# Kernel tuning notes

Hardware: AMD Instinct MI355X
Metric: run time of the kernel (lower is better)

## Reference

```python
import jax, jax.numpy as jnp
import numpy as np

NUM_HEADS = 8


def setup_inputs() -> dict:
    key = jax.random.key(0)
    ks = jax.random.split(key, 6)
    B, E, L = 8, 256, 4096
    top_k = 256
    return {
        "query": jax.random.normal(ks[0], (B, E, L), jnp.float32),
        "keys": jax.random.normal(ks[1], (B, E, L), jnp.float32),
        "values": jax.random.normal(ks[2], (B, E, L), jnp.float32),
        "rand_token_ind": jax.random.randint(ks[3], (B, top_k), 0, L),
        "in_proj_weight": jax.random.normal(ks[4], (3 * E, E), jnp.float32) / np.float32(np.sqrt(E)),
        "in_proj_bias": jnp.zeros((3 * E,), jnp.float32),
        "out_proj_weight": jax.random.normal(ks[5], (E, E), jnp.float32) / np.float32(np.sqrt(E)),
        "out_proj_bias": jnp.zeros((E,), jnp.float32),
        "top_k": top_k,
    }


def _forward(query, keys, values, rand_token_ind, in_proj_weight, in_proj_bias,
             out_proj_weight, out_proj_bias, top_k):
    B, E, Lq = query.shape
    # flatten(2).transpose(-1,-2): channel-first -> [B, L, E]
    q = jnp.swapaxes(query, 1, 2)
    k = jnp.swapaxes(keys, 1, 2)
    v = jnp.swapaxes(values, 1, 2)

    # --- dist_to_random_Q_selection ---
    # random subset of queries, [B, S, E]
    Q_small = jnp.take_along_axis(q, rand_token_ind[:, :, None], axis=1)

    # running min over subset queries of L1 distance (avoids [B,Lk,S,D] blowup)
    def step(min_d, qs):  # qs: [B, E]
        d = jnp.sum(jnp.abs(k - qs[:, None, :]), axis=-1)  # [B, Lk]
        return jnp.minimum(min_d, d), None

    init = jnp.full((B, k.shape[1]), jnp.inf, dtype=k.dtype)
    min_d, _ = jax.lax.scan(step, init, jnp.swapaxes(Q_small, 0, 1))

    # top_k smallest distances, sorted ascending (torch largest=False, sorted=True)
    _, idx = jax.lax.top_k(-min_d, top_k)  # idx: [B, top_k]
    sk = jnp.take_along_axis(k, idx[:, :, None], axis=1)  # [B, top_k, E]
    sv = jnp.take_along_axis(v, idx[:, :, None], axis=1)

    # --- standard torch MultiheadAttention (batch_first) ---
    Wq, Wk, Wv = jnp.split(in_proj_weight, 3, axis=0)
    bq, bk, bv = jnp.split(in_proj_bias, 3, axis=0)
    hd = E // NUM_HEADS
    scale = hd ** -0.5

    def heads(x):
        return x.reshape(x.shape[0], x.shape[1], NUM_HEADS, hd)

    qh = heads(q @ Wq.T + bq) * scale      # [B, Lq, H, hd]
    kh = heads(sk @ Wk.T + bk)             # [B, K,  H, hd]
    vh = heads(sv @ Wv.T + bv)

    scores = jnp.einsum('bqhd,bkhd->bhqk', qh, kh)
    attn = jax.nn.softmax(scores, axis=-1)
    o = jnp.einsum('bhqk,bkhd->bqhd', attn, vh).reshape(B, Lq, E)
    out = o @ out_proj_weight.T + out_proj_bias  # [B, Lq, E]

    # transpose back to original [B, E, Lq] layout
    return jnp.swapaxes(out, 1, 2)


def reference(query, keys, values, rand_token_ind, in_proj_weight, in_proj_bias,
              out_proj_weight, out_proj_bias, top_k):
    return _forward(query, keys, values, rand_token_ind, in_proj_weight,
                    in_proj_bias, out_proj_weight, out_proj_bias, top_k)
```

## Files before the change

### kernel.cpp

```cpp
#include <hip/hip_runtime.h>
#include <math.h>

#define B_SZ   8
#define E_DIM  256
#define L_SEQ  4096
#define S_TOP  256
#define NHEAD  8
#define HD     32
#define NSPLIT 4
#define JSPL   8

typedef __attribute__((ext_vector_type(8))) short bf16x8;
typedef __attribute__((ext_vector_type(4))) float f32x4;

__device__ inline short f2bf(float x) {
    union { float f; unsigned u; } v; v.f = x;
    unsigned r = (v.u + 0x7fff + ((v.u >> 16) & 1)) >> 16;
    return (short)r;
}
__device__ inline float bf2f(short h) {
    union { unsigned u; float f; } c; c.u = ((unsigned)(unsigned short)h) << 16;
    return c.f;
}

__global__ __launch_bounds__(256) void k_prep(const float* __restrict__ query,
                                              const int* __restrict__ ind,
                                              const float* __restrict__ wq,
                                              const float* __restrict__ wo,
                                              float* __restrict__ qs_pack,
                                              short* __restrict__ wqhi,
                                              short* __restrict__ wqlo,
                                              short* __restrict__ wohi,
                                              short* __restrict__ wolo,
                                              short* __restrict__ qhi,
                                              short* __restrict__ qlo) {
    __shared__ float T[64][68];
    const int blk = blockIdx.x;
    if (blk < 2048) {
        int t = blk * 256 + threadIdx.x;
        int e = t & (E_DIM - 1);
        int s = (t >> 8) & (S_TOP - 1);
        int b = t >> 16;
        int idx = ind[b * S_TOP + s];
        qs_pack[t] = query[((size_t)b * E_DIM + e) * L_SEQ + idx];
        return;
    }
    if (blk >= 4096) {
        int t = (blk - 4096) * 256 + threadIdx.x;
        float xq = wq[t];
        short hq = f2bf(xq);
        wqhi[t] = hq;
        wqlo[t] = f2bf(xq - bf2f(hq));
        float xo = wo[t];
        short ho = f2bf(xo);
        wohi[t] = ho;
        wolo[t] = f2bf(xo - bf2f(ho));
        return;
    }
    const int idx = blk - 2048;
    const int b  = idx >> 8;
    const int e0 = ((idx >> 6) & 3) * 64;
    const int l0 = (idx & 63) * 64;
    const float* src = query + ((size_t)b * E_DIM + e0) * L_SEQ + l0;
#pragma unroll
    for (int r = 0; r < 4; ++r) {
        int i2 = threadIdx.x + 256 * r;
        int e = i2 >> 4, l4 = (i2 & 15) * 4;
        *(float4*)&T[e][l4] = *(const float4*)(src + (size_t)e * L_SEQ + l4);
    }
    __syncthreads();
    const int l  = threadIdx.x >> 2;
    const int ec = (threadIdx.x & 3) * 16;
    size_t dst = ((size_t)b * L_SEQ + l0 + l) * E_DIM + e0 + ec;
    bf16x8 h0, h1, lo0, lo1;
#pragma unroll
    for (int k = 0; k < 8; ++k) {
        float x = T[ec + k][l];
        short h = f2bf(x);
        h0[k] = h; lo0[k] = f2bf(x - bf2f(h));
    }
#pragma unroll
    for (int k = 0; k < 8; ++k) {
        float x = T[ec + 8 + k][l];
        short h = f2bf(x);
        h1[k] = h; lo1[k] = f2bf(x - bf2f(h));
    }
    *(bf16x8*)(qhi + dst)     = h0;
    *(bf16x8*)(qhi + dst + 8) = h1;
    *(bf16x8*)(qlo + dst)     = lo0;
    *(bf16x8*)(qlo + dst + 8) = lo1;
}

__global__ __launch_bounds__(256) void k_dist(const float* __restrict__ keys,
                                              const float* __restrict__ qs_pack,
                                              double* __restrict__ minpart) {
    const int b  = blockIdx.z;
    const int ss = blockIdx.y;
    const int l0 = blockIdx.x * 64;
    const int lid = threadIdx.x;
    const int tx = lid & 15;
    const int ty = lid >> 4;
    __shared__ float Ks[32][64];
    __shared__ float Qs[64][36];
    double (*red)[64] = (double(*)[64])&Ks[0][0];

    const float* kb = keys + (size_t)b * E_DIM * L_SEQ + l0;
    const float* qb = qs_pack + ((size_t)b * S_TOP + ss * 64) * E_DIM;

    double d[4][4];
#pragma unroll
    for (int i = 0; i < 4; ++i)
#pragma unroll
        for (int j = 0; j < 4; ++j) d[i][j] = 0.0;

    float4 pk[2], pq[2];
    {
#pragma unroll
        for (int r = 0; r < 2; ++r) {
            int f4 = lid + 256 * r;
            int e  = f4 >> 4, l4 = (f4 & 15) * 4;
            pk[r] = *(const float4*)(kb + (size_t)e * L_SEQ + l4);
            int s  = f4 >> 3, e4 = (f4 & 7) * 4;
            pq[r] = *(const float4*)(qb + (size_t)s * E_DIM + e4);
        }
    }

    for (int c0 = 0; c0 < E_DIM; c0 += 32) {
        __syncthreads();
#pragma unroll
        for (int r = 0; r < 2; ++r) {
            int f4 = lid + 256 * r;
            int e  = f4 >> 4, l4 = (f4 & 15) * 4;
            *(float4*)&Ks[e][l4] = pk[r];
            int s  = f4 >> 3, e4 = (f4 & 7) * 4;
            *(float4*)&Qs[s][e4] = pq[r];
        }
        __syncthreads();
        if (c0 + 32 < E_DIM) {
            const int cn = c0 + 32;
#pragma unroll
            for (int r = 0; r < 2; ++r) {
                int f4 = lid + 256 * r;
                int e  = f4 >> 4, l4 = (f4 & 15) * 4;
                pk[r] = *(const float4*)(kb + (size_t)(cn + e) * L_SEQ + l4);
                int s  = f4 >> 3, e4 = (f4 & 7) * 4;
                pq[r] = *(const float4*)(qb + (size_t)s * E_DIM + cn + e4);
            }
        }

        float cs[4][4] = {};
#pragma unroll
        for (int e4 = 0; e4 < 32; e4 += 4) {
            float qv[4][4];
#pragma unroll
            for (int j = 0; j < 4; ++j) {
                float4 q = *(const float4*)&Qs[ty * 4 + j][e4];
                qv[j][0] = q.x; qv[j][1] = q.y; qv[j][2] = q.z; qv[j][3] = q.w;
            }
#pragma unroll
            for (int ee = 0; ee < 4; ++ee) {
                float kv[4];
#pragma unroll
                for (int i = 0; i < 4; ++i) kv[i] = Ks[e4 + ee][tx * 4 + i];
#pragma unroll
                for (int i = 0; i < 4; ++i)
#pragma unroll
                    for (int j = 0; j < 4; ++j)
                        cs[i][j] += fabsf(kv[i] - qv[j][ee]);
            }
        }
#pragma unroll
        for (int i = 0; i < 4; ++i)
#pragma unroll
            for (int j = 0; j < 4; ++j) d[i][j] += (double)cs[i][j];
    }

    double md[4];
#pragma unroll
    for (int i = 0; i < 4; ++i) {
        double m = d[i][0];
        m = fmin(m, d[i][1]);
        m = fmin(m, d[i][2]);
        m = fmin(m, d[i][3]);
        md[i] = m;
    }
    __syncthreads();
#pragma unroll
    for (int i = 0; i < 4; ++i) red[ty][tx * 4 + i] = md[i];
    __syncthreads();
    if (lid < 64) {
        double m = red[0][lid];
#pragma unroll
        for (int t = 1; t < 16; ++t) m = fmin(m, red[t][lid]);
        minpart[((size_t)(b * NSPLIT + ss)) * L_SEQ + l0 + lid] = m;
    }
}

__global__ __launch_bounds__(256) void k_rankpart(const double* __restrict__ minpart,
                                                  int* __restrict__ rankpart) {
    const int b  = blockIdx.z;
    const int js = blockIdx.y;
    const int l  = blockIdx.x * 256 + threadIdx.x;
    __shared__ double sd[512];
    const double* mp = minpart + (size_t)b * NSPLIT * L_SEQ;
    for (int jj = threadIdx.x; jj < 512; jj += 256) {
        const int j = js * 512 + jj;
        double v = mp[j];
        v = fmin(v, mp[L_SEQ + j]);
        v = fmin(v, mp[2 * L_SEQ + j]);
        v = fmin(v, mp[3 * L_SEQ + j]);
        sd[jj] = v;
    }
    double dl = mp[l];
    dl = fmin(dl, mp[L_SEQ + l]);
    dl = fmin(dl, mp[2 * L_SEQ + l]);
    dl = fmin(dl, mp[3 * L_SEQ + l]);
    __syncthreads();
    const int jbase = js * 512;
    int rank = 0;
#pragma unroll 8
    for (int jj = 0; jj < 512; ++jj) {
        double dj = sd[jj];
        rank += (dj < dl) || (dj == dl && (jbase + jj) < l) ? 1 : 0;
    }
    rankpart[((size_t)(b * JSPL + js)) * L_SEQ + l] = rank;
}

__global__ __launch_bounds__(256) void k_sel(const int* __restrict__ rankpart,
                                             int* __restrict__ sel) {
    const int t = blockIdx.x * 256 + threadIdx.x;
    const int b = t >> 12;
    const int l = t & (L_SEQ - 1);
    int r = 0;
#pragma unroll
    for (int s = 0; s < JSPL; ++s)
        r += rankpart[((size_t)(b * JSPL + s)) * L_SEQ + l];
    if (r < S_TOP) sel[b * S_TOP + r] = l;
}

__global__ __launch_bounds__(256) void k_kvproj2(const float* __restrict__ keys,
                                                 const float* __restrict__ vals,
                                                 const int* __restrict__ sel,
                                                 const float* __restrict__ Wk,
                                                 const float* __restrict__ bk,
                                                 const float* __restrict__ Wv,
                                                 const float* __restrict__ bv,
                                                 short* __restrict__ khb,
                                                 short* __restrict__ vtb) {
    const int b  = blockIdx.z;
    const int f0 = blockIdx.x * 64;
    const int TR = blockIdx.y >> 2;
    const int k0 = (blockIdx.y & 3) * 64;
    const float* src  = TR ? vals : keys;
    const float* W    = TR ? Wv : Wk;
    const float* bias = TR ? bv : bk;
    const int tx = threadIdx.x, ty = threadIdx.y;
    const int lid = ty * 16 + tx;
    __shared__ float As[16][68];
    __shared__ float Ws[16][68];
    float c[4][4] = {};
    const float* sb = src + (size_t)b * E_DIM * L_SEQ;
    const int* selb = sel + b * S_TOP;
    for (int e0 = 0; e0 < E_DIM; e0 += 16) {
        {
            int e  = lid >> 4;
            int k4 = (lid & 15) * 4;
#pragma unroll
            for (int c2 = 0; c2 < 4; ++c2) {
                int kk = k4 + c2;
                As[e][kk] = sb[(size_t)(e0 + e) * L_SEQ + selb[k0 + kk]];
            }
        }
        {
            int f  = lid >> 2;
            int e4 = (lid & 3) * 4;
            float4 w = *(const float4*)(W + (size_t)(f0 + f) * E_DIM + e0 + e4);
            Ws[e4 + 0][f] = w.x; Ws[e4 + 1][f] = w.y;
            Ws[e4 + 2][f] = w.z; Ws[e4 + 3][f] = w.w;
        }
        __syncthreads();
#pragma unroll
        for (int e = 0; e < 16; ++e) {
            float4 a = *(const float4*)&As[e][ty * 4];
            float4 w = *(const float4*)&Ws[e][tx * 4];
            float av[4] = {a.x, a.y, a.z, a.w};
            float wv[4] = {w.x, w.y, w.z, w.w};
#pragma unroll
            for (int i = 0; i < 4; ++i)
#pragma unroll
                for (int j = 0; j < 4; ++j) c[i][j] += av[i] * wv[j];
        }
        __syncthreads();
    }
    if (TR == 0) {
#pragma unroll
        for (int i = 0; i < 4; ++i) {
            short4 o;
            o.x = f2bf(c[i][0] + bias[f0 + tx * 4 + 0]);
            o.y = f2bf(c[i][1] + bias[f0 + tx * 4 + 1]);
            o.z = f2bf(c[i][2] + bias[f0 + tx * 4 + 2]);
            o.w = f2bf(c[i][3] + bias[f0 + tx * 4 + 3]);
            *(short4*)(khb + ((size_t)b * S_TOP + k0 + ty * 4 + i) * E_DIM + f0 + tx * 4) = o;
        }
    } else {
#pragma unroll
        for (int j = 0; j < 4; ++j) {
            const float bvv = bias[f0 + tx * 4 + j];
            short4 o;
            o.x = f2bf(c[0][j] + bvv); o.y = f2bf(c[1][j] + bvv);
            o.z = f2bf(c[2][j] + bvv); o.w = f2bf(c[3][j] + bvv);
            *(short4*)(vtb + ((size_t)b * E_DIM + f0 + tx * 4 + j) * S_TOP + k0 + ty * 4) = o;
        }
    }
}

__global__ __launch_bounds__(256) void k_qgemm(const short* __restrict__ qhi,
                                               const short* __restrict__ qlo,
                                               const short* __restrict__ wqhi,
                                               const short* __restrict__ wqlo,
                                               const float* __restrict__ bias,
                                               short* __restrict__ qhb,
                                               float scale) {
    const int b  = blockIdx.z;
    const int f0 = blockIdx.x * 128;
    const int l0 = blockIdx.y * 128;
    const int lid  = threadIdx.x;
    const int wv   = lid >> 6;
    const int lane = lid & 63;
    const int quad = lane >> 4;
    const int m    = lane & 15;
    const int wf   = wv >> 1;
    const int wl   = wv & 1;

    __shared__ short Awh[128 * 40];
    __shared__ short Awl[128 * 40];
    __shared__ short Bqh[128 * 40];
    __shared__ short Bql[128 * 40];

    const short* wh_g = wqhi + (size_t)f0 * E_DIM;
    const short* wl_g = wqlo + (size_t)f0 * E_DIM;
    const short* qh_g = qhi + ((size_t)b * L_SEQ + l0) * E_DIM;
    const short* ql_g = qlo + ((size_t)b * L_SEQ + l0) * E_DIM;

    f32x4 acc[4][4];
    const f32x4 zero = {0.f, 0.f, 0.f, 0.f};
#pragma unroll
    for (int i = 0; i < 4; ++i)
#pragma unroll
        for (int j = 0; j < 4; ++j) acc[i][j] = zero;

    for (int k0 = 0; k0 < E_DIM; k0 += 32) {
        __syncthreads();
#pragma unroll
        for (int r = 0; r < 2; ++r) {
            int idx = lid + 256 * r;
            int row = idx >> 2;
            int kc  = (idx & 3) * 8;
            *(bf16x8*)&Awh[row * 40 + kc] = *(const bf16x8*)(wh_g + (size_t)row * E_DIM + k0 + kc);
            *(bf16x8*)&Awl[row * 40 + kc] = *(const bf16x8*)(wl_g + (size_t)row * E_DIM + k0 + kc);
            *(bf16x8*)&Bqh[row * 40 + kc] = *(const bf16x8*)(qh_g + (size_t)row * E_DIM + k0 + kc);
            *(bf16x8*)&Bql[row * 40 + kc] = *(const bf16x8*)(ql_g + (size_t)row * E_DIM + k0 + kc);
        }
        __syncthreads();

        bf16x8 ah[4], al[4], bh[4], bl[4];
#pragma unroll
        for (int tf = 0; tf < 4; ++tf) {
            int row = wf * 64 + tf * 16 + m;
            ah[tf] = *(const bf16x8*)&Awh[row * 40 + quad * 8];
            al[tf] = *(const bf16x8*)&Awl[row * 40 + quad * 8];
        }
#pragma unroll
        for (int tl = 0; tl < 4; ++tl) {
            int row = wl * 64 + tl * 16 + m;
            bh[tl] = *(const bf16x8*)&Bqh[row * 40 + quad * 8];
            bl[tl] = *(const bf16x8*)&Bql[row * 40 + quad * 8];
        }
#pragma unroll
        for (int tf = 0; tf < 4; ++tf)
#pragma unroll
            for (int tl = 0; tl < 4; ++tl) {
                acc[tf][tl] = __builtin_amdgcn_mfma_f32_16x16x32_bf16(al[tf], bh[tl], acc[tf][tl], 0, 0, 0);
                acc[tf][tl] = __builtin_amdgcn_mfma_f32_16x16x32_bf16(ah[tf], bl[tl], acc[tf][tl], 0, 0, 0);
                acc[tf][tl] = __builtin_amdgcn_mfma_f32_16x16x32_bf16(ah[tf], bh[tl], acc[tf][tl], 0, 0, 0);
            }
    }

#pragma unroll
    for (int tf = 0; tf < 4; ++tf) {
        const int fb = f0 + wf * 64 + tf * 16 + quad * 4;
        float bv0 = bias[fb + 0], bv1 = bias[fb + 1];
        float bv2 = bias[fb + 2], bv3 = bias[fb + 3];
#pragma unroll
        for (int tl = 0; tl < 4; ++tl) {
            const int l = l0 + wl * 64 + tl * 16 + m;
            short4 o;
            o.x = f2bf(scale * (acc[tf][tl][0] + bv0));
            o.y = f2bf(scale * (acc[tf][tl][1] + bv1));
            o.z = f2bf(scale * (acc[tf][tl][2] + bv2));
            o.w = f2bf(scale * (acc[tf][tl][3] + bv3));
            *(short4*)(qhb + ((size_t)b * L_SEQ + l) * E_DIM + fb) = o;
        }
    }
}

__global__ __launch_bounds__(256) void k_attn(const short* __restrict__ qhb,
                                              const short* __restrict__ khb,
                                              const short* __restrict__ vtb,
                                              short* __restrict__ ohi,
                                              short* __restrict__ olo) {
    __shared__ short P[4][16][264];
    const int b = blockIdx.z, h = blockIdx.y;
    const int wv   = threadIdx.x >> 6;
    const int lane = threadIdx.x & 63;
    const int quad = lane >> 4;
    const int m    = lane & 15;
    const int l0 = blockIdx.x * 64 + wv * 16;

    const short* qp = qhb + ((size_t)b * L_SEQ + l0 + m) * E_DIM + h * HD + quad * 8;
    const bf16x8 qa = *(const bf16x8*)qp;

    const short* kb = khb + (size_t)b * S_TOP * E_DIM + h * HD + quad * 8;
    f32x4 sacc[16];
    const f32x4 zero = {0.f, 0.f, 0.f, 0.f};
#pragma unroll
    for (int t = 0; t < 16; ++t) {
        bf16x8 kf = *(const bf16x8*)(kb + (size_t)(t * 16 + m) * E_DIM);
        sacc[t] = __builtin_amdgcn_mfma_f32_16x16x32_bf16(qa, kf, zero, 0, 0, 0);
    }

    float mx[4], ssum[4];
#pragma unroll
    for (int r = 0; r < 4; ++r) {
        float v = sacc[0][r];
#pragma unroll
        for (int t = 1; t < 16; ++t) v = fmaxf(v, sacc[t][r]);
#pragma unroll
        for (int off = 1; off < 16; off <<= 1) v = fmaxf(v, __shfl_xor(v, off, 16));
        mx[r] = v;
        ssum[r] = 0.f;
    }
#pragma unroll
    for (int t = 0; t < 16; ++t) {
#pragma unroll
        for (int r = 0; r < 4; ++r) {
            float p = __expf(sacc[t][r] - mx[r]);
            ssum[r] += p;
            P[wv][quad * 4 + r][t * 16 + m] = f2bf(p);
        }
    }
#pragma unroll
    for (int r = 0; r < 4; ++r) {
        float v = ssum[r];
#pragma unroll
        for (int off = 1; off < 16; off <<= 1) v += __shfl_xor(v, off, 16);
        ssum[r] = v;
    }

    const short* vb = vtb + ((size_t)b * E_DIM + h * HD) * S_TOP;
    f32x4 oacc[2];
#pragma unroll
    for (int dt = 0; dt < 2; ++dt) {
        f32x4 acc = zero;
#pragma unroll
        for (int k0 = 0; k0 < S_TOP; k0 += 32) {
            bf16x8 pa = *(const bf16x8*)&P[wv][m][k0 + quad * 8];
            bf16x8 vf = *(const bf16x8*)(vb + (size_t)(dt * 16 + m) * S_TOP + k0 + quad * 8);
            acc = __builtin_amdgcn_mfma_f32_16x16x32_bf16(pa, vf, acc, 0, 0, 0);
        }
        oacc[dt] = acc;
    }

    short* oph = ohi + ((size_t)b * L_SEQ + l0) * E_DIM + h * HD;
    short* opl = olo + ((size_t)b * L_SEQ + l0) * E_DIM + h * HD;
#pragma unroll
    for (int r = 0; r < 4; ++r) {
        const float inv = 1.0f / ssum[r];
#pragma unroll
        for (int dt = 0; dt < 2; ++dt) {
            float val = oacc[dt][r] * inv;
            short hh = f2bf(val);
            size_t off = (size_t)(quad * 4 + r) * E_DIM + dt * 16 + m;
            oph[off] = hh;
            opl[off] = f2bf(val - bf2f(hh));
        }
    }
}

__global__ __launch_bounds__(256) void k_ogemm(const short* __restrict__ ohi,
                                               const short* __restrict__ olo,
                                               const short* __restrict__ wohi,
                                               const short* __restrict__ wolo,
                                               const float* __restrict__ bias,
                                               float* __restrict__ out) {
    const int b  = blockIdx.z;
    const int f0 = blockIdx.x * 128;
    const int l0 = blockIdx.y * 128;
    const int lid  = threadIdx.x;
    const int wv   = lid >> 6;
    const int lane = lid & 63;
    const int quad = lane >> 4;
    const int m    = lane & 15;
    const int wl   = wv >> 1;
    const int wf   = wv & 1;

    __shared__ short Aoh[128 * 40];
    __shared__ short Aol[128 * 40];
    __shared__ short Bwh[128 * 40];
    __shared__ short Bwl[128 * 40];

    const short* oh_g = ohi + ((size_t)b * L_SEQ + l0) * E_DIM;
    const short* ol_g = olo + ((size_t)b * L_SEQ + l0) * E_DIM;
    const short* wh_g = wohi + (size_t)f0 * E_DIM;
    const short* wl_g = wolo + (size_t)f0 * E_DIM;

    f32x4 acc[4][4];
    const f32x4 zero = {0.f, 0.f, 0.f, 0.f};
#pragma unroll
    for (int i = 0; i < 4; ++i)
#pragma unroll
        for (int j = 0; j < 4; ++j) acc[i][j] = zero;

    for (int k0 = 0; k0 < E_DIM; k0 += 32) {
        __syncthreads();
#pragma unroll
        for (int r = 0; r < 2; ++r) {
            int idx = lid + 256 * r;
            int row = idx >> 2;
            int kc  = (idx & 3) * 8;
            *(bf16x8*)&Aoh[row * 40 + kc] = *(const bf16x8*)(oh_g + (size_t)row * E_DIM + k0 + kc);
            *(bf16x8*)&Aol[row * 40 + kc] = *(const bf16x8*)(ol_g + (size_t)row * E_DIM + k0 + kc);
            *(bf16x8*)&Bwh[row * 40 + kc] = *(const bf16x8*)(wh_g + (size_t)row * E_DIM + k0 + kc);
            *(bf16x8*)&Bwl[row * 40 + kc] = *(const bf16x8*)(wl_g + (size_t)row * E_DIM + k0 + kc);
        }
        __syncthreads();

        bf16x8 ah[4], al[4], bh[4], bl[4];
#pragma unroll
        for (int tl = 0; tl < 4; ++tl) {
            int row = wl * 64 + tl * 16 + m;
            ah[tl] = *(const bf16x8*)&Aoh[row * 40 + quad * 8];
            al[tl] = *(const bf16x8*)&Aol[row * 40 + quad * 8];
        }
#pragma unroll
        for (int tf = 0; tf < 4; ++tf) {
            int row = wf * 64 + tf * 16 + m;
            bh[tf] = *(const bf16x8*)&Bwh[row * 40 + quad * 8];
            bl[tf] = *(const bf16x8*)&Bwl[row * 40 + quad * 8];
        }
#pragma unroll
        for (int tl = 0; tl < 4; ++tl)
#pragma unroll
            for (int tf = 0; tf < 4; ++tf) {
                acc[tl][tf] = __builtin_amdgcn_mfma_f32_16x16x32_bf16(al[tl], bh[tf], acc[tl][tf], 0, 0, 0);
                acc[tl][tf] = __builtin_amdgcn_mfma_f32_16x16x32_bf16(ah[tl], bl[tf], acc[tl][tf], 0, 0, 0);
                acc[tl][tf] = __builtin_amdgcn_mfma_f32_16x16x32_bf16(ah[tl], bh[tf], acc[tl][tf], 0, 0, 0);
            }
    }

#pragma unroll
    for (int tl = 0; tl < 4; ++tl) {
        const int lb = l0 + wl * 64 + tl * 16 + quad * 4;
#pragma unroll
        for (int tf = 0; tf < 4; ++tf) {
            const int f = f0 + wf * 64 + tf * 16 + m;
            const float bv = bias[f];
            float4 o;
            o.x = acc[tl][tf][0] + bv;
            o.y = acc[tl][tf][1] + bv;
            o.z = acc[tl][tf][2] + bv;
            o.w = acc[tl][tf][3] + bv;
            *(float4*)(out + ((size_t)b * E_DIM + f) * L_SEQ + lb) = o;
        }
    }
}

extern "C" void kernel_launch(void* const* d_in, const int* in_sizes, int n_in,
                              void* d_out, int out_size, void* d_ws, size_t ws_size,
                              hipStream_t stream) {
    const float* query = (const float*)d_in[0];
    const float* keys  = (const float*)d_in[1];
    const float* vals  = (const float*)d_in[2];
    const int*   rind  = (const int*)d_in[3];
    const float* ipw   = (const float*)d_in[4];
    const float* ipb   = (const float*)d_in[5];
    const float* opw   = (const float*)d_in[6];
    const float* opb   = (const float*)d_in[7];
    float* out = (float*)d_out;

    char* ws = (char*)d_ws;
    const size_t MI = 1024 * 1024;
    float*  qs_pack  = (float*)(ws + 0);
    double* minpart  = (double*)(ws + 2 * MI);
    int*    sel      = (int*)   (ws + 3 * MI);
    short*  khb      = (short*) (ws + 4 * MI);
    int*    rankpart = (int*)   (ws + 5 * MI);
    short*  vtb      = (short*) (ws + 6 * MI);
    short*  wqhi     = (short*) (ws + 7 * MI);
    short*  wqlo     = (short*) (ws + 7 * MI + 131072);
    short*  wohi     = (short*) (ws + 7 * MI + 2 * 131072);
    short*  wolo     = (short*) (ws + 7 * MI + 3 * 131072);
    short*  qhb      = (short*) (ws + 8 * MI);
    short*  qhi      = (short*) (ws + 24 * MI);
    short*  qlo      = (short*) (ws + 40 * MI);
    short*  ohi      = (short*) (ws + 24 * MI);
    short*  olo      = (short*) (ws + 40 * MI);

    const float scale = 0.17677669529663687f;

    k_prep<<<dim3(4352), 256, 0, stream>>>(query, rind, ipw, opw, qs_pack,
                                           wqhi, wqlo, wohi, wolo, qhi, qlo);
    k_dist<<<dim3(L_SEQ / 64, NSPLIT, B_SZ), dim3(256), 0, stream>>>(keys, qs_pack, minpart);
    k_rankpart<<<dim3(L_SEQ / 256, JSPL, B_SZ), 256, 0, stream>>>(minpart, rankpart);
    k_sel<<<dim3((B_SZ * L_SEQ) / 256), 256, 0, stream>>>(rankpart, sel);
    k_kvproj2<<<dim3(E_DIM / 64, 2 * (S_TOP / 64), B_SZ), dim3(16, 16), 0, stream>>>(
        keys, vals, sel,
        ipw + (size_t)E_DIM * E_DIM, ipb + E_DIM,
        ipw + (size_t)2 * E_DIM * E_DIM, ipb + 2 * E_DIM,
        khb, vtb);
    k_qgemm<<<dim3(E_DIM / 128, L_SEQ / 128, B_SZ), 256, 0, stream>>>(
        qhi, qlo, wqhi, wqlo, ipb, qhb, scale);
    k_attn<<<dim3(L_SEQ / 64, NHEAD, B_SZ), 256, 0, stream>>>(qhb, khb, vtb, ohi, olo);
    k_ogemm<<<dim3(E_DIM / 128, L_SEQ / 128, B_SZ), 256, 0, stream>>>(
        ohi, olo, wohi, wolo, opb, out);
}
```

Measured before the change: 470.3 us.

## Double-buffer distance kernel tiles via direct global-to-LDS loads

The L1-distance kernel now loads key and query tiles straight into shared memory with global_load_lds, instead of staging them through registers. Shared memory is double-buffered so the next chunk's load is issued while the current chunk is computed. This cuts register pressure and the LDS store instructions. It drops the Qs padding, which may bring back bank conflicts. There is also no explicit wait on the async LDS writes beyond __syncthreads, so correctness depends on the compiler inserting vmcnt waits.

```diff
diff --git a/kernel.cpp b/kernel.cpp
--- a/kernel.cpp
+++ b/kernel.cpp
@@ -12,6 +12,10 @@
 
 typedef __attribute__((ext_vector_type(8))) short bf16x8;
 typedef __attribute__((ext_vector_type(4))) float f32x4;
+
+#define GLDS16(gsrc, ldst) __builtin_amdgcn_global_load_lds( \
+    (const __attribute__((address_space(1))) void*)(gsrc),   \
+    (__attribute__((address_space(3))) void*)(ldst), 16, 0, 0)
 
 __device__ inline short f2bf(float x) {
     union { float f; unsigned u; } v; v.f = x;
@@ -100,9 +104,9 @@
     const int lid = threadIdx.x;
     const int tx = lid & 15;
     const int ty = lid >> 4;
-    __shared__ float Ks[32][64];
-    __shared__ float Qs[64][36];
-    double (*red)[64] = (double(*)[64])&Ks[0][0];
+    __shared__ float Ks[2][32][64];
+    __shared__ float Qs[2][64][32];
+    double (*red)[64] = (double(*)[64])&Ks[0][0][0];
 
     const float* kb = keys + (size_t)b * E_DIM * L_SEQ + l0;
     const float* qb = qs_pack + ((size_t)b * S_TOP + ss * 64) * E_DIM;
@@ -113,38 +117,30 @@
 #pragma unroll
         for (int j = 0; j < 4; ++j) d[i][j] = 0.0;
 
-    float4 pk[2], pq[2];
     {
 #pragma unroll
         for (int r = 0; r < 2; ++r) {
             int f4 = lid + 256 * r;
             int e  = f4 >> 4, l4 = (f4 & 15) * 4;
-            pk[r] = *(const float4*)(kb + (size_t)e * L_SEQ + l4);
+            GLDS16(kb + (size_t)e * L_SEQ + l4, &Ks[0][e][l4]);
             int s  = f4 >> 3, e4 = (f4 & 7) * 4;
-            pq[r] = *(const float4*)(qb + (size_t)s * E_DIM + e4);
-        }
-    }
-
-    for (int c0 = 0; c0 < E_DIM; c0 += 32) {
-        __syncthreads();
-#pragma unroll
-        for (int r = 0; r < 2; ++r) {
-            int f4 = lid + 256 * r;
-            int e  = f4 >> 4, l4 = (f4 & 15) * 4;
-            *(float4*)&Ks[e][l4] = pk[r];
-            int s  = f4 >> 3, e4 = (f4 & 7) * 4;
-            *(float4*)&Qs[s][e4] = pq[r];
-        }
+            GLDS16(qb + (size_t)s * E_DIM + e4, &Qs[0][s][e4]);
+        }
+    }
+
+    int buf = 0;
+    for (int c0 = 0; c0 < E_DIM; c0 += 32, buf ^= 1) {
         __syncthreads();
         if (c0 + 32 < E_DIM) {
             const int cn = c0 + 32;
+            const int nb = buf ^ 1;
 #pragma unroll
             for (int r = 0; r < 2; ++r) {
                 int f4 = lid + 256 * r;
                 int e  = f4 >> 4, l4 = (f4 & 15) * 4;
-                pk[r] = *(const float4*)(kb + (size_t)(cn + e) * L_SEQ + l4);
+                GLDS16(kb + (size_t)(cn + e) * L_SEQ + l4, &Ks[nb][e][l4]);
                 int s  = f4 >> 3, e4 = (f4 & 7) * 4;
-                pq[r] = *(const float4*)(qb + (size_t)s * E_DIM + cn + e4);
+                GLDS16(qb + (size_t)s * E_DIM + cn + e4, &Qs[nb][s][e4]);
             }
         }
 
@@ -154,14 +150,14 @@
             float qv[4][4];
 #pragma unroll
             for (int j = 0; j < 4; ++j) {
-                float4 q = *(const float4*)&Qs[ty * 4 + j][e4];
+                float4 q = *(const float4*)&Qs[buf][ty * 4 + j][e4];
                 qv[j][0] = q.x; qv[j][1] = q.y; qv[j][2] = q.z; qv[j][3] = q.w;
             }
 #pragma unroll
             for (int ee = 0; ee < 4; ++ee) {
                 float kv[4];
 #pragma unroll
-                for (int i = 0; i < 4; ++i) kv[i] = Ks[e4 + ee][tx * 4 + i];
+                for (int i = 0; i < 4; ++i) kv[i] = Ks[buf][e4 + ee][tx * 4 + i];
 #pragma unroll
                 for (int i = 0; i < 4; ++i)
 #pragma unroll
```

New measurement: 439.8 us. 1.07x faster.
